# Kernel tuning notes

Measured on AMD Instinct MI355X. Metric: run time of the kernel, lower is better.

Reference implementation:

```python
import jax, jax.numpy as jnp
import numpy as np

B, DIMS = 8192, 1024
FCN = [DIMS, 2048, 1024, 512, 1]   # self.fcn_dims = [dims] + fcn_dims + [1]
C = 8                               # cluster_num
NLAYERS = len(FCN) - 1              # layer_num = 4


def setup_inputs() -> dict:
    key = jax.random.key(0)
    ks = jax.random.split(key, 2 + 2 * NLAYERS)
    inp = {}
    inp["x"] = jax.random.normal(ks[0], (B, DIMS), dtype=jnp.float32)
    # cluster centers, L2-normalized rows (as in __init__)
    c = jax.random.normal(ks[1], (C, DIMS), dtype=jnp.float32)
    inp["center"] = c / jnp.linalg.norm(c, axis=1, keepdims=True)
    for i in range(NLAYERS):
        fan_in, fan_out = FCN[i], FCN[i + 1]
        # xavier_uniform with relu gain
        gain = float(np.sqrt(2.0))
        bound = gain * float(np.sqrt(6.0 / (fan_in + fan_out)))
        inp[f"w0_{i}"] = jax.random.uniform(ks[2 + 2 * i], (fan_in, fan_out), jnp.float32, -bound, bound)
        inp[f"wc_{i}"] = jax.random.uniform(ks[3 + 2 * i], (C, fan_in, fan_out), jnp.float32, -bound, bound)
    return inp


def _forward(x, center, w0s, wcs):
    # --- router (eval mode: single pass, no center update, no grad) ---
    xd = jax.lax.stop_gradient(x)
    sij = xd @ jax.lax.stop_gradient(center).T          # [B, C]
    router = jnp.argmax(sij, axis=1)                     # [B]
    # --- all cluster towers, gated weights w0 * w_d ---
    h = jnp.broadcast_to(x[None], (C,) + x.shape)        # [C, B, dims]
    for i in range(NLAYERS - 1):
        w = w0s[i][None] * wcs[i]                        # [C, in, out]
        h = jax.nn.relu(jnp.einsum('cbi,cio->cbo', h, w))
    w = w0s[-1][None] * wcs[-1]                          # [C, in, 1]
    h = jax.nn.sigmoid(jnp.einsum('cbi,cio->cbo', h, w))  # [C, B, 1]
    out = jnp.transpose(h[:, :, 0])                      # [B, C]
    # gather per-sample selected cluster output
    return jnp.take_along_axis(out, router[:, None], axis=1)[:, 0]  # [B]


def reference(x, center, w0_0, w0_1, w0_2, w0_3, wc_0, wc_1, wc_2, wc_3):
    w0s = [w0_0, w0_1, w0_2, w0_3]
    wcs = [wc_0, wc_1, wc_2, wc_3]
    return _forward(x, center, w0s, wcs)
```

## Files before the change

### kernel.cpp

```cpp
#include <hip/hip_runtime.h>
#include <hip/hip_bf16.h>

#define B_SZ 8192
#define DIMS 1024
#define CLN 8
#define BM 128
#define PADMAX (B_SZ + CLN * BM)
#define MAX_TILES (B_SZ / BM + CLN)
#define HB 32

typedef __attribute__((ext_vector_type(8))) __bf16 bf16x8;
typedef __attribute__((ext_vector_type(8))) short short8;
typedef __attribute__((ext_vector_type(4))) short short4v;
typedef __attribute__((ext_vector_type(4))) float f32x4;

__device__ __forceinline__ short f2bf(float f) {
  __hip_bfloat16 h = __float2bfloat16(f);
  return __builtin_bit_cast(short, h);
}
__device__ __forceinline__ float bf2f(short s) {
  unsigned u = ((unsigned)(unsigned short)s) << 16;
  return __builtin_bit_cast(float, u);
}

__device__ __forceinline__ void gl_lds16(const short* g, short* l) {
  __builtin_amdgcn_global_load_lds(
      (const __attribute__((address_space(1))) unsigned int*)(unsigned long long)(uintptr_t)g,
      (__attribute__((address_space(3))) unsigned int*)(unsigned long long)(uintptr_t)l,
      16, 0, 0);
}

__global__ void router_kernel(const float* __restrict__ x, const float* __restrict__ center,
                              int* __restrict__ router, short* __restrict__ xb) {
  const int tid = threadIdx.x;
  const int lane = tid & 63;
  const int w = tid >> 6;
  const int s = blockIdx.x * 4 + w;
  const float4* xr = (const float4*)(x + (size_t)s * DIMS);
  float4 xv[4];
#pragma unroll
  for (int j = 0; j < 4; ++j) xv[j] = xr[j * 64 + lane];
  if (xb) {
    short* xbr = xb + (size_t)s * DIMS;
#pragma unroll
    for (int j = 0; j < 4; ++j) {
      short4v sv;
      sv[0] = f2bf(xv[j].x); sv[1] = f2bf(xv[j].y);
      sv[2] = f2bf(xv[j].z); sv[3] = f2bf(xv[j].w);
      *(short4v*)(xbr + j * 256 + lane * 4) = sv;
    }
  }
  float p[CLN];
#pragma unroll
  for (int c = 0; c < CLN; ++c) {
    const float4* cr = (const float4*)(center + (size_t)c * DIMS);
    float acc = 0.f;
#pragma unroll
    for (int j = 0; j < 4; ++j) {
      float4 cv = cr[j * 64 + lane];
      acc += xv[j].x * cv.x + xv[j].y * cv.y + xv[j].z * cv.z + xv[j].w * cv.w;
    }
    p[c] = acc;
  }
#pragma unroll
  for (int c = 0; c < CLN; ++c) {
#pragma unroll
    for (int m = 1; m < 64; m <<= 1) p[c] += __shfl_xor(p[c], m);
  }
  if (lane == 0) {
    int best = 0; float bv = p[0];
#pragma unroll
    for (int c = 1; c < CLN; ++c) { if (p[c] > bv) { bv = p[c]; best = c; } }
    router[s] = best;
  }
}

__global__ void hist_kernel(const int* __restrict__ router, int* __restrict__ blockcnt) {
  __shared__ int bins[CLN];
  const int t = threadIdx.x;
  if (t < CLN) bins[t] = 0;
  __syncthreads();
  const int c = router[blockIdx.x * 256 + t];
  atomicAdd(&bins[c], 1);
  __syncthreads();
  if (t < CLN) blockcnt[blockIdx.x * CLN + t] = bins[t];
}

__global__ void scan_kernel(const int* __restrict__ blockcnt, int* __restrict__ counts,
                            int* __restrict__ pstart, int* __restrict__ meta,
                            int* __restrict__ tile_c, int* __restrict__ tile_r,
                            int* __restrict__ blockbase) {
  __shared__ int cnt[HB * CLN];
  __shared__ int base[HB * CLN];
  const int t = threadIdx.x;
  cnt[t] = blockcnt[t];
  __syncthreads();
  if (t == 0) {
    int ps = 0, nt = 0;
    for (int c = 0; c < CLN; ++c) {
      int tot = 0;
      for (int b = 0; b < HB; ++b) tot += cnt[b * CLN + c];
      pstart[c] = ps;
      counts[c] = tot;
      int run = ps;
      for (int b = 0; b < HB; ++b) { base[b * CLN + c] = run; run += cnt[b * CLN + c]; }
      const int tiles = (tot + BM - 1) / BM;
      for (int i = 0; i < tiles; ++i) { tile_c[nt] = c; tile_r[nt] = ps + i * BM; ++nt; }
      ps += tiles * BM;
    }
    pstart[CLN] = ps;
    meta[0] = nt;
    meta[1] = ps;
  }
  __syncthreads();
  blockbase[t] = base[t];
}

__global__ void scatter_kernel(const int* __restrict__ router, const int* __restrict__ blockbase,
                               int* __restrict__ order) {
  __shared__ int cur[CLN];
  const int t = threadIdx.x;
  if (t < CLN) cur[t] = 0;
  __syncthreads();
  const int s = blockIdx.x * 256 + t;
  const int c = router[s];
  const int pos = blockbase[blockIdx.x * CLN + c] + atomicAdd(&cur[c], 1);
  order[pos] = s;
}

__global__ void fillpad_kernel(const int* __restrict__ counts, const int* __restrict__ pstart,
                               int* __restrict__ order) {
  const int p = blockIdx.x * blockDim.x + threadIdx.x;
  if (p >= PADMAX) return;
#pragma unroll
  for (int c = 0; c < CLN; ++c) {
    if (p >= pstart[c] && p < pstart[c + 1]) {
      const int idx = p - pstart[c];
      if (idx >= counts[c]) order[p] = order[pstart[c]];
      break;
    }
  }
}

template <int K, int N>
__global__ void gate_kernel(const float* __restrict__ w0, const float* __restrict__ wc,
                            short* __restrict__ gwt) {
  const int k0 = blockIdx.x * 32;
  const int n0 = blockIdx.y * 64;
  const int c = blockIdx.z;
  __shared__ short t[32 * 65];
  const int tid = threadIdx.x;
  const int lk = tid >> 4;
  const int ln = (tid & 15) * 4;
  const float* w0p = w0 + (size_t)k0 * N + n0;
  const float* wcp = wc + (size_t)c * K * N + (size_t)k0 * N + n0;
#pragma unroll
  for (int i = 0; i < 2; ++i) {
    const int k = lk + i * 16;
    float4 a = *(const float4*)(w0p + (size_t)k * N + ln);
    float4 b = *(const float4*)(wcp + (size_t)k * N + ln);
    short* d = &t[k * 65 + ln];
    d[0] = f2bf(a.x * b.x); d[1] = f2bf(a.y * b.y);
    d[2] = f2bf(a.z * b.z); d[3] = f2bf(a.w * b.w);
  }
  __syncthreads();
  const int wn = tid >> 2;
  const int wk = (tid & 3) * 8;
  short8 v;
#pragma unroll
  for (int j = 0; j < 8; ++j) v[j] = t[(wk + j) * 65 + wn];
  *(short8*)(gwt + ((size_t)c * N + n0 + wn) * K + k0 + wk) = v;
}

template <int K, int N, bool GATHER>
__global__ void gemm_async(const short* __restrict__ Abase, const short* __restrict__ gwt,
                           short* __restrict__ Aout, const int* __restrict__ order,
                           const int* __restrict__ tile_c, const int* __restrict__ tile_r,
                           const int* __restrict__ meta) {
  const int bt = blockIdx.x;
  if (bt >= meta[0]) return;
  const int cl = tile_c[bt];
  const int row0 = tile_r[bt];
  const int n0 = blockIdx.y * 128;

  __shared__ __align__(16) short As[128 * 32];
  __shared__ __align__(16) short Bs[128 * 32];

  const int tid = threadIdx.x;
  const int lane = tid & 63;
  const int w = tid >> 6;
  const int wm = w >> 1;
  const int wn = w & 1;

  const int lrow = lane >> 2;
  const int kofs = (lane & 3) << 3;
  const short* ga0;
  const short* ga1;
  if (GATHER) {
    ga0 = Abase + (size_t)order[row0 + w * 16 + lrow] * K + kofs;
    ga1 = Abase + (size_t)order[row0 + 64 + w * 16 + lrow] * K + kofs;
  } else {
    ga0 = Abase + (size_t)(row0 + w * 16 + lrow) * K + kofs;
    ga1 = ga0 + (size_t)64 * K;
  }
  const short* gb0 = gwt + ((size_t)cl * N + n0 + w * 16 + lrow) * K + kofs;
  const short* gb1 = gb0 + (size_t)64 * K;
  short* lA0 = &As[w * 16 * 32];
  short* lA1 = &As[(64 + w * 16) * 32];
  short* lB0 = &Bs[w * 16 * 32];
  short* lB1 = &Bs[(64 + w * 16) * 32];

  f32x4 acc[4][4] = {};
  const int arL = wm * 64 + (lane & 15);
  const int bcL = wn * 64 + (lane & 15);
  const int kq = (lane >> 4) << 3;

  for (int kb = 0; kb < K; kb += 32) {
    __syncthreads();
    gl_lds16(ga0 + kb, lA0);
    gl_lds16(ga1 + kb, lA1);
    gl_lds16(gb0 + kb, lB0);
    gl_lds16(gb1 + kb, lB1);
    __syncthreads();

    short8 af[4], bfr[4];
#pragma unroll
    for (int mi = 0; mi < 4; ++mi) af[mi] = *(const short8*)&As[(arL + mi * 16) * 32 + kq];
#pragma unroll
    for (int ni = 0; ni < 4; ++ni) bfr[ni] = *(const short8*)&Bs[(bcL + ni * 16) * 32 + kq];
#pragma unroll
    for (int mi = 0; mi < 4; ++mi) {
#pragma unroll
      for (int ni = 0; ni < 4; ++ni) {
        acc[mi][ni] = __builtin_amdgcn_mfma_f32_16x16x32_bf16(
            __builtin_bit_cast(bf16x8, af[mi]), __builtin_bit_cast(bf16x8, bfr[ni]),
            acc[mi][ni], 0, 0, 0);
      }
    }
  }

  const int er = (lane >> 4) << 2;
  const int ec = lane & 15;
#pragma unroll
  for (int mi = 0; mi < 4; ++mi) {
#pragma unroll
    for (int ni = 0; ni < 4; ++ni) {
#pragma unroll
      for (int r = 0; r < 4; ++r) {
        float vv = fmaxf(acc[mi][ni][r], 0.f);
        const int row = row0 + wm * 64 + mi * 16 + er + r;
        const int col = n0 + wn * 64 + ni * 16 + ec;
        Aout[(size_t)row * N + col] = f2bf(vv);
      }
    }
  }
}

template <int K, int N, bool GATHER>
__global__ void gemm_layer(const float* __restrict__ Xf, const short* __restrict__ Ain,
                           const float* __restrict__ w0, const float* __restrict__ wc,
                           short* __restrict__ Aout,
                           const int* __restrict__ order,
                           const int* __restrict__ tile_c, const int* __restrict__ tile_r,
                           const int* __restrict__ meta) {
  const int bt = blockIdx.x;
  if (bt >= meta[0]) return;
  const int cl = tile_c[bt];
  const int row0 = tile_r[bt];
  const int n0 = blockIdx.y * 128;

  __shared__ __align__(16) short As[128 * 40];
  __shared__ __align__(16) short Bs[128 * 40];

  const int tid = threadIdx.x;
  const int lane = tid & 63;
  const int wm = (tid >> 6) >> 1;
  const int wn = (tid >> 6) & 1;

  f32x4 acc[4][4] = {};

  const int arow = tid >> 2;
  const int akseg = (tid & 3) << 3;
  const int bn = tid & 127;
  const int bkq = (tid >> 7) << 3;

  const float* xr0 = nullptr; const float* xr1 = nullptr;
  const short* ar0 = nullptr; const short* ar1 = nullptr;
  if (GATHER) {
    xr0 = Xf + (size_t)order[row0 + arow] * K + akseg;
    xr1 = Xf + (size_t)order[row0 + arow + 64] * K + akseg;
  } else {
    ar0 = Ain + (size_t)(row0 + arow) * K + akseg;
    ar1 = Ain + (size_t)(row0 + arow + 64) * K + akseg;
  }
  const float* w0p = w0 + n0 + bn;
  const float* wcp = wc + (size_t)cl * K * N + n0 + bn;

  for (int kb = 0; kb < K; kb += 32) {
    __syncthreads();
    if (GATHER) {
      float4 a = *(const float4*)(xr0 + kb);
      float4 b = *(const float4*)(xr0 + kb + 4);
      short8 v;
      v[0] = f2bf(a.x); v[1] = f2bf(a.y); v[2] = f2bf(a.z); v[3] = f2bf(a.w);
      v[4] = f2bf(b.x); v[5] = f2bf(b.y); v[6] = f2bf(b.z); v[7] = f2bf(b.w);
      *(short8*)&As[arow * 40 + akseg] = v;
      a = *(const float4*)(xr1 + kb);
      b = *(const float4*)(xr1 + kb + 4);
      v[0] = f2bf(a.x); v[1] = f2bf(a.y); v[2] = f2bf(a.z); v[3] = f2bf(a.w);
      v[4] = f2bf(b.x); v[5] = f2bf(b.y); v[6] = f2bf(b.z); v[7] = f2bf(b.w);
      *(short8*)&As[(arow + 64) * 40 + akseg] = v;
    } else {
      *(short8*)&As[arow * 40 + akseg] = *(const short8*)(ar0 + kb);
      *(short8*)&As[(arow + 64) * 40 + akseg] = *(const short8*)(ar1 + kb);
    }
#pragma unroll
    for (int half = 0; half < 2; ++half) {
      const int kk = bkq + half * 16;
      short8 v;
#pragma unroll
      for (int j = 0; j < 8; ++j) {
        const size_t off = (size_t)(kb + kk + j) * N;
        v[j] = f2bf(w0p[off] * wcp[off]);
      }
      *(short8*)&Bs[bn * 40 + kk] = v;
    }
    __syncthreads();

    const int arL = wm * 64 + (lane & 15);
    const int kq = (lane >> 4) << 3;
    const int bcL = wn * 64 + (lane & 15);
    short8 af[4], bfr[4];
#pragma unroll
    for (int mi = 0; mi < 4; ++mi) af[mi] = *(const short8*)&As[(arL + mi * 16) * 40 + kq];
#pragma unroll
    for (int ni = 0; ni < 4; ++ni) bfr[ni] = *(const short8*)&Bs[(bcL + ni * 16) * 40 + kq];
#pragma unroll
    for (int mi = 0; mi < 4; ++mi) {
#pragma unroll
      for (int ni = 0; ni < 4; ++ni) {
        acc[mi][ni] = __builtin_amdgcn_mfma_f32_16x16x32_bf16(
            __builtin_bit_cast(bf16x8, af[mi]), __builtin_bit_cast(bf16x8, bfr[ni]),
            acc[mi][ni], 0, 0, 0);
      }
    }
  }

  const int er = (lane >> 4) << 2;
  const int ec = lane & 15;
#pragma unroll
  for (int mi = 0; mi < 4; ++mi) {
#pragma unroll
    for (int ni = 0; ni < 4; ++ni) {
#pragma unroll
      for (int r = 0; r < 4; ++r) {
        float vv = fmaxf(acc[mi][ni][r], 0.f);
        const int row = row0 + wm * 64 + mi * 16 + er + r;
        const int col = n0 + wn * 64 + ni * 16 + ec;
        Aout[(size_t)row * N + col] = f2bf(vv);
      }
    }
  }
}

__global__ void layer3_kernel(const short* __restrict__ h2, const float* __restrict__ w03,
                              const float* __restrict__ wc3, const int* __restrict__ order,
                              const int* __restrict__ pstart, const int* __restrict__ meta,
                              float* __restrict__ out) {
  const int tid = threadIdx.x;
  const int lane = tid & 63;
  const int w = tid >> 6;
  const int r = blockIdx.x * 4 + w;
  if (r >= meta[1]) return;
  int c = 0;
#pragma unroll
  for (int i = 1; i < CLN; ++i) { if (r >= pstart[i]) c = i; }
  const short* hr = h2 + (size_t)r * 512;
  const int k0 = lane * 8;
  const short8 hv = *(const short8*)(hr + k0);
  const float* wcr = wc3 + c * 512;
  float part = 0.f;
#pragma unroll
  for (int j = 0; j < 8; ++j) part += bf2f(hv[j]) * w03[k0 + j] * wcr[k0 + j];
  for (int off = 32; off; off >>= 1) part += __shfl_down(part, off);
  if (lane == 0) out[order[r]] = 1.f / (1.f + expf(-part));
}

extern "C" void kernel_launch(void* const* d_in, const int* in_sizes, int n_in,
                              void* d_out, int out_size, void* d_ws, size_t ws_size,
                              hipStream_t stream) {
  const float* x = (const float*)d_in[0];
  const float* center = (const float*)d_in[1];
  const float* w0s[4]; const float* wcs[4];
  if (in_sizes[3] == 8 * in_sizes[2]) {
    for (int i = 0; i < 4; ++i) { w0s[i] = (const float*)d_in[2 + 2 * i]; wcs[i] = (const float*)d_in[3 + 2 * i]; }
  } else {
    for (int i = 0; i < 4; ++i) { w0s[i] = (const float*)d_in[2 + i]; wcs[i] = (const float*)d_in[6 + i]; }
  }
  float* out = (float*)d_out;
  char* ws = (char*)d_ws;
  int* counts    = (int*)(ws + 0);
  int* pstart    = (int*)(ws + 128);
  int* meta      = (int*)(ws + 192);
  int* tile_c    = (int*)(ws + 256);
  int* tile_r    = (int*)(ws + 1024);
  int* blockcnt  = (int*)(ws + 1536);
  int* blockbase = (int*)(ws + 2560);
  int* router    = (int*)(ws + 4096);
  int* order     = (int*)(ws + 4096 + 4 * B_SZ);

  const size_t GW_BYTES = (size_t)CLN * 2048 * 1024 * 2;
  const size_t H0_BYTES = (size_t)PADMAX * 2048 * 2;
  const size_t H1_BYTES = (size_t)PADMAX * 1024 * 2;
  const size_t NEED = 131072 + GW_BYTES + H0_BYTES + H1_BYTES;
  const bool fast = (ws_size >= NEED);

  short* gw = (short*)(ws + 131072);
  short* h0 = (short*)(ws + 131072 + GW_BYTES);
  short* h1 = (short*)(ws + 131072 + GW_BYTES + H0_BYTES);
  short* xb = fast ? h1 : nullptr;

  router_kernel<<<B_SZ / 4, 256, 0, stream>>>(x, center, router, xb);
  hist_kernel<<<HB, 256, 0, stream>>>(router, blockcnt);
  scan_kernel<<<1, HB * CLN, 0, stream>>>(blockcnt, counts, pstart, meta, tile_c, tile_r, blockbase);
  scatter_kernel<<<HB, 256, 0, stream>>>(router, blockbase, order);
  fillpad_kernel<<<PADMAX / 256, 256, 0, stream>>>(counts, pstart, order);

  if (fast) {
    short* h2 = h0;

    gate_kernel<1024, 2048><<<dim3(32, 32, CLN), 256, 0, stream>>>(w0s[0], wcs[0], gw);
    gemm_async<1024, 2048, true><<<dim3(MAX_TILES, 16), 256, 0, stream>>>(
        xb, gw, h0, order, tile_c, tile_r, meta);
    gate_kernel<2048, 1024><<<dim3(64, 16, CLN), 256, 0, stream>>>(w0s[1], wcs[1], gw);
    gemm_async<2048, 1024, false><<<dim3(MAX_TILES, 8), 256, 0, stream>>>(
        h0, gw, h1, order, tile_c, tile_r, meta);
    gate_kernel<1024, 512><<<dim3(32, 8, CLN), 256, 0, stream>>>(w0s[2], wcs[2], gw);
    gemm_async<1024, 512, false><<<dim3(MAX_TILES, 4), 256, 0, stream>>>(
        h1, gw, h2, order, tile_c, tile_r, meta);
    layer3_kernel<<<(PADMAX + 3) / 4, 256, 0, stream>>>(h2, w0s[3], wcs[3], order, pstart, meta, out);
  } else {
    short* f0 = (short*)(ws + 131072);
    short* f1 = f0 + (size_t)PADMAX * 2048;
    short* f2 = f1 + (size_t)PADMAX * 1024;
    gemm_layer<1024, 2048, true><<<dim3(MAX_TILES, 16), 256, 0, stream>>>(
        x, nullptr, w0s[0], wcs[0], f0, order, tile_c, tile_r, meta);
    gemm_layer<2048, 1024, false><<<dim3(MAX_TILES, 8), 256, 0, stream>>>(
        nullptr, f0, w0s[1], wcs[1], f1, order, tile_c, tile_r, meta);
    gemm_layer<1024, 512, false><<<dim3(MAX_TILES, 4), 256, 0, stream>>>(
        nullptr, f1, w0s[2], wcs[2], f2, order, tile_c, tile_r, meta);
    layer3_kernel<<<(PADMAX + 3) / 4, 256, 0, stream>>>(f2, w0s[3], wcs[3], order, pstart, meta, out);
  }
}
```

Measured before the change: 406.6 us.

## Fuse routing sort into one kernel, batch gating, and widen GEMM K-step

Replaces the hist/scan/scatter/fillpad kernels with a single 1024-thread sort kernel that uses ballot-based counting and scatter. All three gate (w0*wc) conversions move into one launch when the workspace is large enough. The GEMM grid is flattened to 1D, and each main-loop iteration now loads two 32-wide K slabs, halving the number of barrier pairs. The aim is to cut launch count and per-iteration sync overhead, at the cost of a larger workspace requirement and serialized work in the single-block sort.

```diff
diff --git a/kernel.cpp b/kernel.cpp
--- a/kernel.cpp
+++ b/kernel.cpp
@@ -7,7 +7,6 @@
 #define BM 128
 #define PADMAX (B_SZ + CLN * BM)
 #define MAX_TILES (B_SZ / BM + CLN)
-#define HB 32
 
 typedef __attribute__((ext_vector_type(8))) __bf16 bf16x8;
 typedef __attribute__((ext_vector_type(8))) short short8;
@@ -75,80 +74,77 @@
   }
 }
 
-__global__ void hist_kernel(const int* __restrict__ router, int* __restrict__ blockcnt) {
+__global__ void sort_kernel(const int* __restrict__ router, int* __restrict__ counts,
+                            int* __restrict__ pstart, int* __restrict__ meta,
+                            int* __restrict__ tile_c, int* __restrict__ tile_r,
+                            int* __restrict__ order) {
   __shared__ int bins[CLN];
+  __shared__ int cur[CLN];
+  __shared__ int ps_s[CLN + 1];
   const int t = threadIdx.x;
+  const int lane = t & 63;
   if (t < CLN) bins[t] = 0;
   __syncthreads();
-  const int c = router[blockIdx.x * 256 + t];
-  atomicAdd(&bins[c], 1);
-  __syncthreads();
-  if (t < CLN) blockcnt[blockIdx.x * CLN + t] = bins[t];
-}
-
-__global__ void scan_kernel(const int* __restrict__ blockcnt, int* __restrict__ counts,
-                            int* __restrict__ pstart, int* __restrict__ meta,
-                            int* __restrict__ tile_c, int* __restrict__ tile_r,
-                            int* __restrict__ blockbase) {
-  __shared__ int cnt[HB * CLN];
-  __shared__ int base[HB * CLN];
-  const int t = threadIdx.x;
-  cnt[t] = blockcnt[t];
+  int myc[8];
+#pragma unroll
+  for (int j = 0; j < 8; ++j) myc[j] = router[t + 1024 * j];
+#pragma unroll
+  for (int j = 0; j < 8; ++j) {
+#pragma unroll
+    for (int c = 0; c < CLN; ++c) {
+      unsigned long long m = __ballot(myc[j] == c);
+      if (lane == 0 && m) atomicAdd(&bins[c], __popcll(m));
+    }
+  }
   __syncthreads();
   if (t == 0) {
     int ps = 0, nt = 0;
     for (int c = 0; c < CLN; ++c) {
-      int tot = 0;
-      for (int b = 0; b < HB; ++b) tot += cnt[b * CLN + c];
-      pstart[c] = ps;
-      counts[c] = tot;
-      int run = ps;
-      for (int b = 0; b < HB; ++b) { base[b * CLN + c] = run; run += cnt[b * CLN + c]; }
+      const int tot = bins[c];
+      counts[c] = tot; pstart[c] = ps; ps_s[c] = ps; cur[c] = 0;
       const int tiles = (tot + BM - 1) / BM;
       for (int i = 0; i < tiles; ++i) { tile_c[nt] = c; tile_r[nt] = ps + i * BM; ++nt; }
       ps += tiles * BM;
     }
-    pstart[CLN] = ps;
-    meta[0] = nt;
-    meta[1] = ps;
+    pstart[CLN] = ps; ps_s[CLN] = ps; meta[0] = nt; meta[1] = ps;
   }
   __syncthreads();
-  blockbase[t] = base[t];
-}
-
-__global__ void scatter_kernel(const int* __restrict__ router, const int* __restrict__ blockbase,
-                               int* __restrict__ order) {
-  __shared__ int cur[CLN];
-  const int t = threadIdx.x;
-  if (t < CLN) cur[t] = 0;
+#pragma unroll
+  for (int j = 0; j < 8; ++j) {
+    const int s = t + 1024 * j;
+    const int c = myc[j];
+    int pos = 0;
+#pragma unroll
+    for (int cc = 0; cc < CLN; ++cc) {
+      unsigned long long m = __ballot(c == cc);
+      int b = 0;
+      if (lane == 0 && m) b = atomicAdd(&cur[cc], __popcll(m));
+      b = __shfl(b, 0);
+      if (c == cc) pos = ps_s[cc] + b + __popcll(m & ((1ull << lane) - 1ull));
+    }
+    order[pos] = s;
+  }
   __syncthreads();
-  const int s = blockIdx.x * 256 + t;
-  const int c = router[s];
-  const int pos = blockbase[blockIdx.x * CLN + c] + atomicAdd(&cur[c], 1);
-  order[pos] = s;
-}
-
-__global__ void fillpad_kernel(const int* __restrict__ counts, const int* __restrict__ pstart,
-                               int* __restrict__ order) {
-  const int p = blockIdx.x * blockDim.x + threadIdx.x;
-  if (p >= PADMAX) return;
-#pragma unroll
-  for (int c = 0; c < CLN; ++c) {
-    if (p >= pstart[c] && p < pstart[c + 1]) {
-      const int idx = p - pstart[c];
-      if (idx >= counts[c]) order[p] = order[pstart[c]];
-      break;
+  for (int p = t; p < PADMAX; p += 1024) {
+#pragma unroll
+    for (int c = 0; c < CLN; ++c) {
+      if (p >= ps_s[c] && p < ps_s[c + 1]) {
+        if (p - ps_s[c] >= bins[c]) order[p] = order[ps_s[c]];
+        break;
+      }
     }
   }
 }
 
 template <int K, int N>
-__global__ void gate_kernel(const float* __restrict__ w0, const float* __restrict__ wc,
-                            short* __restrict__ gwt) {
-  const int k0 = blockIdx.x * 32;
-  const int n0 = blockIdx.y * 64;
-  const int c = blockIdx.z;
-  __shared__ short t[32 * 65];
+__device__ __forceinline__ void gate_body(const float* __restrict__ w0,
+                                          const float* __restrict__ wc,
+                                          short* __restrict__ gwt, int bx, short* t) {
+  constexpr int NK = K / 32, NN = N / 64;
+  const int c = bx / (NK * NN);
+  const int rem = bx % (NK * NN);
+  const int k0 = (rem % NK) * 32;
+  const int n0 = (rem / NK) * 64;
   const int tid = threadIdx.x;
   const int lk = tid >> 4;
   const int ln = (tid & 15) * 4;
@@ -172,19 +168,39 @@
   *(short8*)(gwt + ((size_t)c * N + n0 + wn) * K + k0 + wk) = v;
 }
 
+__global__ void gate_all(const float* __restrict__ w00, const float* __restrict__ wc0, short* g0,
+                         const float* __restrict__ w01, const float* __restrict__ wc1, short* g1,
+                         const float* __restrict__ w02, const float* __restrict__ wc2, short* g2) {
+  __shared__ short t[32 * 65];
+  const int bx = blockIdx.x;
+  if (bx < 8192)       gate_body<1024, 2048>(w00, wc0, g0, bx, t);
+  else if (bx < 16384) gate_body<2048, 1024>(w01, wc1, g1, bx - 8192, t);
+  else                 gate_body<1024, 512>(w02, wc2, g2, bx - 16384, t);
+}
+
+template <int K, int N>
+__global__ void gate_kernel(const float* __restrict__ w0, const float* __restrict__ wc,
+                            short* __restrict__ gwt) {
+  __shared__ short t[32 * 65];
+  gate_body<K, N>(w0, wc, gwt, blockIdx.x, t);
+}
+
 template <int K, int N, bool GATHER>
 __global__ void gemm_async(const short* __restrict__ Abase, const short* __restrict__ gwt,
                            short* __restrict__ Aout, const int* __restrict__ order,
                            const int* __restrict__ tile_c, const int* __restrict__ tile_r,
                            const int* __restrict__ meta) {
-  const int bt = blockIdx.x;
+  constexpr int NT = N / 128;
+  const int bt = blockIdx.x / NT;
   if (bt >= meta[0]) return;
+  const int n0 = (blockIdx.x % NT) * 128;
   const int cl = tile_c[bt];
   const int row0 = tile_r[bt];
-  const int n0 = blockIdx.y * 128;
-
-  __shared__ __align__(16) short As[128 * 32];
-  __shared__ __align__(16) short Bs[128 * 32];
+
+  __shared__ __align__(16) short As0[128 * 32];
+  __shared__ __align__(16) short As1[128 * 32];
+  __shared__ __align__(16) short Bs0[128 * 32];
+  __shared__ __align__(16) short Bs1[128 * 32];
 
   const int tid = threadIdx.x;
   const int lane = tid & 63;
@@ -205,36 +221,51 @@
   }
   const short* gb0 = gwt + ((size_t)cl * N + n0 + w * 16 + lrow) * K + kofs;
   const short* gb1 = gb0 + (size_t)64 * K;
-  short* lA0 = &As[w * 16 * 32];
-  short* lA1 = &As[(64 + w * 16) * 32];
-  short* lB0 = &Bs[w * 16 * 32];
-  short* lB1 = &Bs[(64 + w * 16) * 32];
+  short* lo = (short*)((char*)nullptr);
+  (void)lo;
+  short* lA0a = &As0[w * 16 * 32];
+  short* lA0b = &As0[(64 + w * 16) * 32];
+  short* lA1a = &As1[w * 16 * 32];
+  short* lA1b = &As1[(64 + w * 16) * 32];
+  short* lB0a = &Bs0[w * 16 * 32];
+  short* lB0b = &Bs0[(64 + w * 16) * 32];
+  short* lB1a = &Bs1[w * 16 * 32];
+  short* lB1b = &Bs1[(64 + w * 16) * 32];
 
   f32x4 acc[4][4] = {};
   const int arL = wm * 64 + (lane & 15);
   const int bcL = wn * 64 + (lane & 15);
   const int kq = (lane >> 4) << 3;
 
-  for (int kb = 0; kb < K; kb += 32) {
+  for (int kb = 0; kb < K; kb += 64) {
     __syncthreads();
-    gl_lds16(ga0 + kb, lA0);
-    gl_lds16(ga1 + kb, lA1);
-    gl_lds16(gb0 + kb, lB0);
-    gl_lds16(gb1 + kb, lB1);
+    gl_lds16(ga0 + kb, lA0a);
+    gl_lds16(ga1 + kb, lA0b);
+    gl_lds16(ga0 + kb + 32, lA1a);
+    gl_lds16(ga1 + kb + 32, lA1b);
+    gl_lds16(gb0 + kb, lB0a);
+    gl_lds16(gb1 + kb, lB0b);
+    gl_lds16(gb0 + kb + 32, lB1a);
+    gl_lds16(gb1 + kb + 32, lB1b);
     __syncthreads();
 
-    short8 af[4], bfr[4];
-#pragma unroll
-    for (int mi = 0; mi < 4; ++mi) af[mi] = *(const short8*)&As[(arL + mi * 16) * 32 + kq];
-#pragma unroll
-    for (int ni = 0; ni < 4; ++ni) bfr[ni] = *(const short8*)&Bs[(bcL + ni * 16) * 32 + kq];
-#pragma unroll
-    for (int mi = 0; mi < 4; ++mi) {
-#pragma unroll
-      for (int ni = 0; ni < 4; ++ni) {
-        acc[mi][ni] = __builtin_amdgcn_mfma_f32_16x16x32_bf16(
-            __builtin_bit_cast(bf16x8, af[mi]), __builtin_bit_cast(bf16x8, bfr[ni]),
-            acc[mi][ni], 0, 0, 0);
+#pragma unroll
+    for (int h = 0; h < 2; ++h) {
+      const short* Ap = h ? As1 : As0;
+      const short* Bp = h ? Bs1 : Bs0;
+      short8 af[4], bfr[4];
+#pragma unroll
+      for (int mi = 0; mi < 4; ++mi) af[mi] = *(const short8*)&Ap[(arL + mi * 16) * 32 + kq];
+#pragma unroll
+      for (int ni = 0; ni < 4; ++ni) bfr[ni] = *(const short8*)&Bp[(bcL + ni * 16) * 32 + kq];
+#pragma unroll
+      for (int mi = 0; mi < 4; ++mi) {
+#pragma unroll
+        for (int ni = 0; ni < 4; ++ni) {
+          acc[mi][ni] = __builtin_amdgcn_mfma_f32_16x16x32_bf16(
+              __builtin_bit_cast(bf16x8, af[mi]), __builtin_bit_cast(bf16x8, bfr[ni]),
+              acc[mi][ni], 0, 0, 0);
+        }
       }
     }
   }
@@ -399,50 +430,68 @@
   }
   float* out = (float*)d_out;
   char* ws = (char*)d_ws;
-  int* counts    = (int*)(ws + 0);
-  int* pstart    = (int*)(ws + 128);
-  int* meta      = (int*)(ws + 192);
-  int* tile_c    = (int*)(ws + 256);
-  int* tile_r    = (int*)(ws + 1024);
-  int* blockcnt  = (int*)(ws + 1536);
-  int* blockbase = (int*)(ws + 2560);
-  int* router    = (int*)(ws + 4096);
-  int* order     = (int*)(ws + 4096 + 4 * B_SZ);
-
-  const size_t GW_BYTES = (size_t)CLN * 2048 * 1024 * 2;
-  const size_t H0_BYTES = (size_t)PADMAX * 2048 * 2;
-  const size_t H1_BYTES = (size_t)PADMAX * 1024 * 2;
-  const size_t NEED = 131072 + GW_BYTES + H0_BYTES + H1_BYTES;
-  const bool fast = (ws_size >= NEED);
-
-  short* gw = (short*)(ws + 131072);
-  short* h0 = (short*)(ws + 131072 + GW_BYTES);
-  short* h1 = (short*)(ws + 131072 + GW_BYTES + H0_BYTES);
-  short* xb = fast ? h1 : nullptr;
-
-  router_kernel<<<B_SZ / 4, 256, 0, stream>>>(x, center, router, xb);
-  hist_kernel<<<HB, 256, 0, stream>>>(router, blockcnt);
-  scan_kernel<<<1, HB * CLN, 0, stream>>>(blockcnt, counts, pstart, meta, tile_c, tile_r, blockbase);
-  scatter_kernel<<<HB, 256, 0, stream>>>(router, blockbase, order);
-  fillpad_kernel<<<PADMAX / 256, 256, 0, stream>>>(counts, pstart, order);
-
-  if (fast) {
+  int* counts = (int*)(ws + 0);
+  int* pstart = (int*)(ws + 128);
+  int* meta   = (int*)(ws + 192);
+  int* tile_c = (int*)(ws + 256);
+  int* tile_r = (int*)(ws + 1024);
+  int* router = (int*)(ws + 4096);
+  int* order  = (int*)(ws + 4096 + 4 * B_SZ);
+
+  const size_t GW0 = (size_t)CLN * 1024 * 2048 * 2;
+  const size_t GW1 = (size_t)CLN * 2048 * 1024 * 2;
+  const size_t GW2 = (size_t)CLN * 1024 * 512 * 2;
+  const size_t H0B = (size_t)PADMAX * 2048 * 2;
+  const size_t H1B = (size_t)PADMAX * 1024 * 2;
+  const size_t NEED_A = 131072 + GW0 + GW1 + GW2 + H0B + H1B;
+  const size_t NEED_B = 131072 + GW1 + H0B + H1B;
+  const int tier = (ws_size >= NEED_A) ? 0 : (ws_size >= NEED_B) ? 1 : 2;
+
+  if (tier == 0) {
+    short* gw0 = (short*)(ws + 131072);
+    short* gw1 = (short*)(ws + 131072 + GW0);
+    short* gw2 = (short*)(ws + 131072 + GW0 + GW1);
+    short* h0  = (short*)(ws + 131072 + GW0 + GW1 + GW2);
+    short* h1  = (short*)(ws + 131072 + GW0 + GW1 + GW2 + H0B);
+    short* xb  = h1;
+    short* h2  = h0;
+
+    router_kernel<<<B_SZ / 4, 256, 0, stream>>>(x, center, router, xb);
+    sort_kernel<<<1, 1024, 0, stream>>>(router, counts, pstart, meta, tile_c, tile_r, order);
+    gate_all<<<18432, 256, 0, stream>>>(w0s[0], wcs[0], gw0, w0s[1], wcs[1], gw1,
+                                        w0s[2], wcs[2], gw2);
+    gemm_async<1024, 2048, true><<<MAX_TILES * 16, 256, 0, stream>>>(
+        xb, gw0, h0, order, tile_c, tile_r, meta);
+    gemm_async<2048, 1024, false><<<MAX_TILES * 8, 256, 0, stream>>>(
+        h0, gw1, h1, order, tile_c, tile_r, meta);
+    gemm_async<1024, 512, false><<<MAX_TILES * 4, 256, 0, stream>>>(
+        h1, gw2, h2, order, tile_c, tile_r, meta);
+    layer3_kernel<<<(PADMAX + 3) / 4, 256, 0, stream>>>(h2, w0s[3], wcs[3], order, pstart, meta, out);
+  } else if (tier == 1) {
+    short* gw = (short*)(ws + 131072);
+    short* h0 = (short*)(ws + 131072 + GW1);
+    short* h1 = (short*)(ws + 131072 + GW1 + H0B);
+    short* xb = h1;
     short* h2 = h0;
 
-    gate_kernel<1024, 2048><<<dim3(32, 32, CLN), 256, 0, stream>>>(w0s[0], wcs[0], gw);
-    gemm_async<1024, 2048, true><<<dim3(MAX_TILES, 16), 256, 0, stream>>>(
+    router_kernel<<<B_SZ / 4, 256, 0, stream>>>(x, center, router, xb);
+    sort_kernel<<<1, 1024, 0, stream>>>(router, counts, pstart, meta, tile_c, tile_r, order);
+    gate_kernel<1024, 2048><<<8192, 256, 0, stream>>>(w0s[0], wcs[0], gw);
+    gemm_async<1024, 2048, true><<<MAX_TILES * 16, 256, 0, stream>>>(
         xb, gw, h0, order, tile_c, tile_r, meta);
-    gate_kernel<2048, 1024><<<dim3(64, 16, CLN), 256, 0, stream>>>(w0s[1], wcs[1], gw);
-    gemm_async<2048, 1024, false><<<dim3(MAX_TILES, 8), 256, 0, stream>>>(
+    gate_kernel<2048, 1024><<<8192, 256, 0, stream>>>(w0s[1], wcs[1], gw);
+    gemm_async<2048, 1024, false><<<MAX_TILES * 8, 256, 0, stream>>>(
         h0, gw, h1, order, tile_c, tile_r, meta);
-    gate_kernel<1024, 512><<<dim3(32, 8, CLN), 256, 0, stream>>>(w0s[2], wcs[2], gw);
-    gemm_async<1024, 512, false><<<dim3(MAX_TILES, 4), 256, 0, stream>>>(
+    gate_kernel<1024, 512><<<2048, 256, 0, stream>>>(w0s[2], wcs[2], gw);
+    gemm_async<1024, 512, false><<<MAX_TILES * 4, 256, 0, stream>>>(
         h1, gw, h2, order, tile_c, tile_r, meta);
     layer3_kernel<<<(PADMAX + 3) / 4, 256, 0, stream>>>(h2, w0s[3], wcs[3], order, pstart, meta, out);
   } else {
     short* f0 = (short*)(ws + 131072);
     short* f1 = f0 + (size_t)PADMAX * 2048;
     short* f2 = f1 + (size_t)PADMAX * 1024;
+    router_kernel<<<B_SZ / 4, 256, 0, stream>>>(x, center, router, nullptr);
+    sort_kernel<<<1, 1024, 0, stream>>>(router, counts, pstart, meta, tile_c, tile_r, order);
     gemm_layer<1024, 2048, true><<<dim3(MAX_TILES, 16), 256, 0, stream>>>(
         x, nullptr, w0s[0], wcs[0], f0, order, tile_c, tile_r, meta);
     gemm_layer<2048, 1024, false><<<dim3(MAX_TILES, 8), 256, 0, stream>>>(
```

New measurement: 404.4 us. About the same (-0.5%).
